# Kernel tuning notes

Measured on AMD Instinct MI355X. Metric: run time of the kernel, lower is better.

Reference implementation:

```python
import jax, jax.numpy as jnp
import numpy as np

B, N_MODES, N_CLASSES = 200000, 64, 10
HBAR = 2.0


def setup_inputs() -> dict:
    key = jax.random.key(0)
    k1, k2, k3, k4 = jax.random.split(key, 4)
    twoN = 2 * N_MODES
    x = jax.random.normal(k1, (B, N_MODES), dtype=jnp.float32)
    # Ansatz (learned Gaussian channel): symplectic-like matrix S and displacement d.
    S = jax.random.normal(k2, (twoN, twoN), dtype=jnp.float32) * (1.0 / np.sqrt(twoN))
    d = jax.random.normal(k3, (twoN,), dtype=jnp.float32)
    bias = jnp.zeros((N_MODES,), dtype=jnp.float32)
    W = jax.random.normal(k4, (N_CLASSES, N_MODES), dtype=jnp.float32) * (1.0 / np.sqrt(N_MODES))
    b = jnp.zeros((N_CLASSES,), dtype=jnp.float32)
    return {"x": x, "S": S, "d": d, "bias": bias, "W": W, "b": b}


def reference(x, S, d, bias, W, b):
    # Vacuum mean vector is zero; displacing mode i by alpha = x_i/sqrt(2*hbar)
    # shifts the x-quadrature (even indices, xpxp ordering) by sqrt(2*hbar)*Re(alpha) = x_i.
    Bn = x.shape[0]
    twoN = 2 * x.shape[1]
    mu = jnp.zeros((Bn, twoN), dtype=x.dtype).at[:, ::2].set(x)  # [B, 2N]
    # Ansatz: affine symplectic map mu' = S mu + d (cov transform S cov S^T does
    # not affect the expectation-value homodyne readout mu_x).
    mu_out = mu @ S.T + d  # [B, 2N]
    # Homodyne x-quadrature readout per mode + bias.
    readout = mu_out[:, ::2] + bias  # [B, N]
    return readout @ W.T + b  # [B, n_classes]
```

## Files before the change

### kernel.cpp

```cpp
#include <hip/hip_runtime.h>

#define NM 64
#define NC 10

__global__ __launch_bounds__(640) void cv2d_precompute(
    const float* __restrict__ S,
    const float* __restrict__ d,
    const float* __restrict__ bias,
    const float* __restrict__ W,
    const float* __restrict__ bvec,
    float* __restrict__ ws)
{
    const int t = threadIdx.x;
    const int twoN = 2 * NM;
    if (t < NM * NC) {
        const int m = t / NC;
        const int c = t - m * NC;
        float acc = 0.f;
        #pragma unroll
        for (int k = 0; k < NM; ++k) {
            acc += S[(2 * k) * twoN + 2 * m] * W[c * NM + k];
        }
        ws[m * NC + c] = acc;
    }
    if (t < NC) {
        float acc = bvec[t];
        #pragma unroll
        for (int k = 0; k < NM; ++k) {
            acc += (d[2 * k] + bias[k]) * W[t * NM + k];
        }
        ws[NM * NC + t] = acc;
    }
}

__global__ __launch_bounds__(256) void cv2d_main(
    const float* __restrict__ x,
    const float* __restrict__ Mc,
    float* __restrict__ out,
    int Bn)
{
    const int row = blockIdx.x * 256 + threadIdx.x;
    if (row >= Bn) return;

    const float4* __restrict__ xr = (const float4*)(x + (size_t)row * NM);

    float acc[NC];
    #pragma unroll
    for (int c = 0; c < NC; ++c) acc[c] = Mc[NM * NC + c];

    #pragma unroll
    for (int q = 0; q < NM / 4; ++q) {
        const float4 v = xr[q];
        #pragma unroll
        for (int c = 0; c < NC; ++c) {
            acc[c] += v.x * Mc[(4 * q + 0) * NC + c];
            acc[c] += v.y * Mc[(4 * q + 1) * NC + c];
            acc[c] += v.z * Mc[(4 * q + 2) * NC + c];
            acc[c] += v.w * Mc[(4 * q + 3) * NC + c];
        }
    }

    float2* __restrict__ o = (float2*)(out + (size_t)row * NC);
    #pragma unroll
    for (int c = 0; c < NC; c += 2) {
        o[c / 2] = make_float2(acc[c], acc[c + 1]);
    }
}

extern "C" void kernel_launch(void* const* d_in, const int* in_sizes, int n_in,
                              void* d_out, int out_size, void* d_ws, size_t ws_size,
                              hipStream_t stream) {
    const float* x    = (const float*)d_in[0];
    const float* S    = (const float*)d_in[1];
    const float* d    = (const float*)d_in[2];
    const float* bias = (const float*)d_in[3];
    const float* W    = (const float*)d_in[4];
    const float* bvec = (const float*)d_in[5];
    float* out = (float*)d_out;
    float* ws  = (float*)d_ws;

    const int Bn = in_sizes[0] / NM;

    cv2d_precompute<<<1, 640, 0, stream>>>(S, d, bias, W, bvec, ws);

    const int grid = (Bn + 255) / 256;
    cv2d_main<<<grid, 256, 0, stream>>>(x, ws, out, Bn);
}
```

Before: 106.9 us.

## Fuse weight-folding precompute into main kernel with per-block shared-memory matrix

```diff
diff --git a/kernel.cpp b/kernel.cpp
--- a/kernel.cpp
+++ b/kernel.cpp
@@ -2,69 +2,67 @@
 
 #define NM 64
 #define NC 10
+#define TWO_N 128
 
-__global__ __launch_bounds__(640) void cv2d_precompute(
+
+__global__ __launch_bounds__(256) void cv2d_fused(
+    const float* __restrict__ x,
     const float* __restrict__ S,
-    const float* __restrict__ d,
+    const float* __restrict__ dvec,
     const float* __restrict__ bias,
     const float* __restrict__ W,
     const float* __restrict__ bvec,
-    float* __restrict__ ws)
+    float* __restrict__ out,
+    int Bn)
 {
+    __shared__ __align__(16) float Ms[NC][NM];
+    __shared__ float c0s[NC];
     const int t = threadIdx.x;
-    const int twoN = 2 * NM;
-    if (t < NM * NC) {
-        const int m = t / NC;
-        const int c = t - m * NC;
+
+    for (int e = t; e < NM * NC; e += 256) {
+        const int c = e >> 6;
+        const int m = e & 63;
         float acc = 0.f;
         #pragma unroll
-        for (int k = 0; k < NM; ++k) {
-            acc += S[(2 * k) * twoN + 2 * m] * W[c * NM + k];
-        }
-        ws[m * NC + c] = acc;
+        for (int k = 0; k < NM; ++k)
+            acc += S[(2 * k) * TWO_N + 2 * m] * W[c * NM + k];
+        Ms[c][m] = acc;
     }
     if (t < NC) {
         float acc = bvec[t];
         #pragma unroll
-        for (int k = 0; k < NM; ++k) {
-            acc += (d[2 * k] + bias[k]) * W[t * NM + k];
-        }
-        ws[NM * NC + t] = acc;
+        for (int k = 0; k < NM; ++k)
+            acc += (dvec[2 * k] + bias[k]) * W[t * NM + k];
+        c0s[t] = acc;
     }
-}
+    __syncthreads();
 
-__global__ __launch_bounds__(256) void cv2d_main(
-    const float* __restrict__ x,
-    const float* __restrict__ Mc,
-    float* __restrict__ out,
-    int Bn)
-{
-    const int row = blockIdx.x * 256 + threadIdx.x;
+    const int row = blockIdx.x * 256 + t;
     if (row >= Bn) return;
 
     const float4* __restrict__ xr = (const float4*)(x + (size_t)row * NM);
 
     float acc[NC];
     #pragma unroll
-    for (int c = 0; c < NC; ++c) acc[c] = Mc[NM * NC + c];
+    for (int c = 0; c < NC; ++c) acc[c] = c0s[c];
 
     #pragma unroll
     for (int q = 0; q < NM / 4; ++q) {
         const float4 v = xr[q];
         #pragma unroll
         for (int c = 0; c < NC; ++c) {
-            acc[c] += v.x * Mc[(4 * q + 0) * NC + c];
-            acc[c] += v.y * Mc[(4 * q + 1) * NC + c];
-            acc[c] += v.z * Mc[(4 * q + 2) * NC + c];
-            acc[c] += v.w * Mc[(4 * q + 3) * NC + c];
+            const float4 mm = *(const float4*)&Ms[c][4 * q];
+            acc[c] += v.x * mm.x;
+            acc[c] += v.y * mm.y;
+            acc[c] += v.z * mm.z;
+            acc[c] += v.w * mm.w;
         }
     }
 
     float2* __restrict__ o = (float2*)(out + (size_t)row * NC);
     #pragma unroll
-    for (int c = 0; c < NC; c += 2) {
+    for (int c = 0; c < NC; c += 2)
         o[c / 2] = make_float2(acc[c], acc[c + 1]);
-    }
 }
 
 extern "C" void kernel_launch(void* const* d_in, const int* in_sizes, int n_in,
@@ -77,12 +75,9 @@
     const float* W    = (const float*)d_in[4];
     const float* bvec = (const float*)d_in[5];
     float* out = (float*)d_out;
-    float* ws  = (float*)d_ws;
 
     const int Bn = in_sizes[0] / NM;
 
-    cv2d_precompute<<<1, 640, 0, stream>>>(S, d, bias, W, bvec, ws);
-
     const int grid = (Bn + 255) / 256;
-    cv2d_main<<<grid, 256, 0, stream>>>(x, ws, out, Bn);
+    cv2d_fused<<<grid, 256, 0, stream>>>(x, S, d, bias, W, bvec, out, Bn);
 }
```

Result: slower. 110.1 us (+3.0%).
